# Performance work log

Measured on AMD Instinct MI355X. Metric: run time of the kernel, lower is better.

## Reference

```python
import jax, jax.numpy as jnp
import numpy as np

N, E = 50000, 800000
D, DE = 128, 64
BN_EPS = 1e-5


def _bn(h, gamma, beta):
    # BatchNorm1d in training mode: biased batch statistics over the node axis
    mu = jnp.mean(h, axis=0)
    var = jnp.var(h, axis=0)
    return (h - mu) * jax.lax.rsqrt(var + BN_EPS) * gamma + beta


def setup_inputs() -> dict:
    key = jax.random.key(0)
    ks = jax.random.split(key, 12)
    s = lambda d: 1.0 / np.sqrt(d)
    return {
        "x": jax.random.normal(ks[0], (N, D), jnp.float32),
        "edge_index": jax.random.randint(ks[1], (2, E), 0, N, jnp.int64),
        "edge_attr_processed": jax.random.normal(ks[2], (E, DE), jnp.float32),
        # GINEConv edge linear: edge_dim -> node_dim
        "We": jax.random.uniform(ks[3], (D, DE), jnp.float32, -s(DE), s(DE)),
        "be": jnp.zeros((D,), jnp.float32),
        # MLP: Linear(D, 2D) -> BN(2D) -> ReLU -> Linear(2D, D)
        "W1": jax.random.uniform(ks[4], (2 * D, D), jnp.float32, -s(D), s(D)),
        "b1": jnp.zeros((2 * D,), jnp.float32),
        "g1": jnp.ones((2 * D,), jnp.float32),
        "beta1": jnp.zeros((2 * D,), jnp.float32),
        "W2": jax.random.uniform(ks[5], (D, 2 * D), jnp.float32, -s(2 * D), s(2 * D)),
        "b2": jnp.zeros((D,), jnp.float32),
        # outer BatchNorm(D)
        "g2": jnp.ones((D,), jnp.float32),
        "beta2": jnp.zeros((D,), jnp.float32),
        # GINE trainable eps (init 0.0)
        "eps": jnp.zeros((), jnp.float32),
    }


def reference(x, edge_index, edge_attr_processed, We, be, W1, b1, g1, beta1,
              W2, b2, g2, beta2, eps):
    src, dst = edge_index[0], edge_index[1]
    # GINEConv message: ReLU(x_j + Lin(edge_attr)); gather + edge add + relu
    msg = jax.nn.relu(x[src] + edge_attr_processed @ We.T + be)  # [E, D]
    # scatter-add aggregation at destination nodes
    agg = jax.ops.segment_sum(msg, dst, num_segments=x.shape[0])  # [N, D]
    h = (1.0 + eps) * x + agg
    # MLP: Linear -> BN -> ReLU -> Linear
    h = jax.nn.relu(_bn(h @ W1.T + b1, g1, beta1)) @ W2.T + b2
    # outer BN -> ReLU (dropout is identity at inference)
    return jax.nn.relu(_bn(h, g2, beta2))
```

## Files before the change

kernel.cpp:

```cpp
#include <hip/hip_runtime.h>
#include <stdint.h>
#include <stddef.h>


#define NN 50000
#define EE 800000
#define DD 128
#define DE 64
#define H1 256
#define NGRP 3125

typedef __attribute__((ext_vector_type(8))) short short8;
typedef __attribute__((ext_vector_type(4))) float floatx4;

__device__ __forceinline__ short f2bf(float f) {
    union { float f; uint32_t u; } v; v.f = f;
    return (short)((v.u + 0x7FFFu + ((v.u >> 16) & 1u)) >> 16);
}
__device__ __forceinline__ float bf2f(uint16_t u) {
    union { uint32_t u; float f; } v; v.u = (uint32_t)u << 16;
    return v.f;
}

__global__ __launch_bounds__(256) void swz_all_kernel(
    const float* __restrict__ We, const float* __restrict__ W1,
    const float* __restrict__ W2, short* __restrict__ dst) {
    int idx = blockIdx.x * 256 + threadIdx.x;
    if (idx >= 73728) return;
    const float* src; int KC, K, local; short* dp; bool perm = false;
    if (idx < 8192)       { src = We; KC = 2; K = 64;  local = idx;          dp = dst; }
    else if (idx < 40960) { src = W1; KC = 4; K = 128; local = idx - 8192;  dp = dst + 8192; perm = true; }
    else                  { src = W2; KC = 8; K = 256; local = idx - 40960; dp = dst + 40960; }
    int j = local & 7;
    int lane = (local >> 3) & 63;
    int f = local >> 9;
    int kc = f % KC;
    int nt = f / KC;
    int n = nt * 16 + (lane & 15);
    int k = kc * 32 + ((lane >> 4) & 3) * 8 + j;
    if (perm) k = ((k & 7) << 4) | (k >> 3);
    dp[local] = f2bf(src[(size_t)n * K + k]);
}

__global__ __launch_bounds__(256) void count_kernel(const int* __restrict__ ei,
                                                    uint32_t* __restrict__ deg) {
    int e = blockIdx.x * 256 + threadIdx.x;
    atomicAdd(&deg[ei[EE + e]], 1u);
}

__global__ __launch_bounds__(256) void scan1_kernel(const uint32_t* __restrict__ deg,
                                                    uint32_t* __restrict__ partial) {
    __shared__ uint32_t ls[256];
    int i = blockIdx.x * 256 + threadIdx.x;
    ls[threadIdx.x] = deg[i];
    __syncthreads();
    for (int s = 128; s > 0; s >>= 1) {
        if (threadIdx.x < s) ls[threadIdx.x] += ls[threadIdx.x + s];
        __syncthreads();
    }
    if (threadIdx.x == 0) partial[blockIdx.x] = ls[0];
}

__global__ __launch_bounds__(256) void scan2_kernel(uint32_t* __restrict__ partial) {
    __shared__ uint32_t ls[196];
    if (threadIdx.x < 196) ls[threadIdx.x] = partial[threadIdx.x];
    __syncthreads();
    if (threadIdx.x == 0) {
        uint32_t run = 0;
        for (int i = 0; i < 196; ++i) { uint32_t t = ls[i]; ls[i] = run; run += t; }
    }
    __syncthreads();
    if (threadIdx.x < 196) partial[threadIdx.x] = ls[threadIdx.x];
}

__global__ __launch_bounds__(256) void scan3_kernel(const uint32_t* __restrict__ deg,
                                                    const uint32_t* __restrict__ partial,
                                                    uint32_t* __restrict__ base,
                                                    uint32_t* __restrict__ cursor) {
    __shared__ uint32_t ls[256];
    int i = blockIdx.x * 256 + threadIdx.x;
    uint32_t v = (i < NN) ? deg[i] : 0u;
    ls[threadIdx.x] = v;
    __syncthreads();
    for (int off = 1; off < 256; off <<= 1) {
        uint32_t t = (threadIdx.x >= off) ? ls[threadIdx.x - off] : 0u;
        __syncthreads();
        ls[threadIdx.x] += t;
        __syncthreads();
    }
    if (i < NN) {
        uint32_t b = partial[blockIdx.x] + ls[threadIdx.x] - v;
        base[i] = b;
        cursor[i] = b;
    } else if (i == NN) {
        base[NN] = EE;
    }
}

__global__ __launch_bounds__(256) void pos_kernel(const int* __restrict__ ei,
                                                  uint32_t* __restrict__ cursor,
                                                  uint32_t* __restrict__ pos) {
    int e = blockIdx.x * 256 + threadIdx.x;
    pos[e] = atomicAdd(&cursor[ei[EE + e]], 1u);
}

#define EDGE_GPW 5
__global__ __launch_bounds__(256) void edge_kernel(
    const float* __restrict__ x,
    const int* __restrict__ ei,
    const float* __restrict__ ea,
    const short* __restrict__ weswz,
    const float* __restrict__ be,
    const uint32_t* __restrict__ pos,
    uint16_t* __restrict__ msg)
{
    const int wave = threadIdx.x >> 6;
    const int lane = threadIdx.x & 63;
    const int l16 = lane & 15;
    const int q = lane >> 4;

    const short8* wp = (const short8*)weswz;
    short8 bfr[16];
#pragma unroll
    for (int f = 0; f < 16; ++f) bfr[f] = wp[f * 64 + lane];
    float bev[8];
#pragma unroll
    for (int t = 0; t < 8; ++t) bev[t] = be[t * 16 + l16];

    const int gbase = (blockIdx.x * 4 + wave) * EDGE_GPW;
    for (int g = 0; g < EDGE_GPW; ++g) {
        const int e0 = (gbase + g) * 16;
        const float* earow = ea + (size_t)(e0 + l16) * DE + q * 8;
        floatx4 p0 = *(const floatx4*)(earow);
        floatx4 p1 = *(const floatx4*)(earow + 4);
        floatx4 p2 = *(const floatx4*)(earow + 32);
        floatx4 p3 = *(const floatx4*)(earow + 36);
        short8 af0, af1;
#pragma unroll
        for (int j = 0; j < 4; ++j) {
            af0[j]     = f2bf(p0[j]);
            af0[j + 4] = f2bf(p1[j]);
            af1[j]     = f2bf(p2[j]);
            af1[j + 4] = f2bf(p3[j]);
        }
        floatx4 acc[8];
#pragma unroll
        for (int t = 0; t < 8; ++t) {
            floatx4 z = {0.f, 0.f, 0.f, 0.f};
            z = __builtin_amdgcn_mfma_f32_16x16x32_bf16(af0, bfr[t * 2], z, 0, 0, 0);
            acc[t] = __builtin_amdgcn_mfma_f32_16x16x32_bf16(af1, bfr[t * 2 + 1], z, 0, 0, 0);
        }
        int   sidx[4];
        uint32_t ppv[4];
#pragma unroll
        for (int r = 0; r < 4; ++r) {
            sidx[r] = ei[e0 + q * 4 + r];
            ppv[r]  = pos[e0 + q * 4 + r];
        }
#pragma unroll
        for (int r = 0; r < 4; ++r) {
            const float* xr = x + (size_t)sidx[r] * DD + l16;
            uint32_t pk[4];
#pragma unroll
            for (int tt = 0; tt < 4; ++tt) {
                float v0 = fmaxf(acc[2 * tt][r]     + bev[2 * tt]     + xr[(2 * tt) * 16], 0.f);
                float v1 = fmaxf(acc[2 * tt + 1][r] + bev[2 * tt + 1] + xr[(2 * tt + 1) * 16], 0.f);
                pk[tt] = (uint32_t)(uint16_t)f2bf(v0) | ((uint32_t)(uint16_t)f2bf(v1) << 16);
            }
            uint4 val = {pk[0], pk[1], pk[2], pk[3]};
            *(uint4*)(msg + (size_t)ppv[r] * DD + l16 * 8) = val;
        }
    }
}

__global__ __launch_bounds__(256) void reduce_kernel(
    const uint16_t* __restrict__ msg,
    const uint32_t* __restrict__ basep,
    const float* __restrict__ x,
    const float* __restrict__ epsp,
    uint16_t* __restrict__ hbf)
{
    const int n = blockIdx.x * 4 + (threadIdx.x >> 6);
    const int lane = threadIdx.x & 63;
    const uint32_t b0 = basep[n];
    const uint32_t d = basep[n + 1] - b0;
    const uint32_t* mp = (const uint32_t*)msg + (size_t)b0 * 64 + lane;
    float s0a = 0.f, s1a = 0.f, s0b = 0.f, s1b = 0.f;
    float s0c = 0.f, s1c = 0.f, s0d = 0.f, s1d = 0.f;
    uint32_t i = 0;
    for (; i + 4 <= d; i += 4) {
        uint32_t u0 = mp[(size_t)(i + 0) * 64];
        uint32_t u1 = mp[(size_t)(i + 1) * 64];
        uint32_t u2 = mp[(size_t)(i + 2) * 64];
        uint32_t u3 = mp[(size_t)(i + 3) * 64];
        s0a += bf2f((uint16_t)(u0 & 0xFFFFu)); s1a += bf2f((uint16_t)(u0 >> 16));
        s0b += bf2f((uint16_t)(u1 & 0xFFFFu)); s1b += bf2f((uint16_t)(u1 >> 16));
        s0c += bf2f((uint16_t)(u2 & 0xFFFFu)); s1c += bf2f((uint16_t)(u2 >> 16));
        s0d += bf2f((uint16_t)(u3 & 0xFFFFu)); s1d += bf2f((uint16_t)(u3 >> 16));
    }
    for (; i < d; ++i) {
        uint32_t u = mp[(size_t)i * 64];
        s0a += bf2f((uint16_t)(u & 0xFFFFu)); s1a += bf2f((uint16_t)(u >> 16));
    }
    float s0 = (s0a + s0b) + (s0c + s0d);
    float s1 = (s1a + s1b) + (s1c + s1d);
    const float c1 = 1.0f + epsp[0];
    const int o0 = (((lane * 2) & 7) << 4) + (lane >> 2);
    const float* xrow = x + (size_t)n * DD;
    float xa = xrow[o0];
    float xb = xrow[o0 + 16];
    uint32_t pk = (uint32_t)(uint16_t)f2bf(c1 * xa + s0) |
                  ((uint32_t)(uint16_t)f2bf(c1 * xb + s1) << 16);
    ((uint32_t*)hbf)[n * 64 + lane] = pk;
}

__global__ __launch_bounds__(256) void gemm1_kernel(
    const uint16_t* __restrict__ hbf,
    const short* __restrict__ w1swz,
    const float* __restrict__ b1,
    uint16_t* __restrict__ t1,
    float* __restrict__ gsum,
    float* __restrict__ gsq)
{
    __shared__ float ls[H1];
    __shared__ float ls2[H1];
    const int tid = threadIdx.x;
    ls[tid] = 0.f; ls2[tid] = 0.f;
    __syncthreads();

    const int wave = tid >> 6;
    const int lane = tid & 63;
    const int l16 = lane & 15;
    const int q = lane >> 4;
    const short8* wp = (const short8*)w1swz;

    const int grp = blockIdx.x * 4 + wave;
    if (grp < NGRP) {
        const int n0 = grp * 16;
        const uint16_t* hr = hbf + (size_t)(n0 + l16) * DD + q * 8;
        short8 af[4];
#pragma unroll
        for (int kc = 0; kc < 4; ++kc) af[kc] = *(const short8*)(hr + kc * 32);
#pragma unroll
        for (int nt = 0; nt < 16; ++nt) {
            floatx4 acc = {0.f, 0.f, 0.f, 0.f};
#pragma unroll
            for (int kc = 0; kc < 4; ++kc)
                acc = __builtin_amdgcn_mfma_f32_16x16x32_bf16(
                    af[kc], wp[(nt * 4 + kc) * 64 + lane], acc, 0, 0, 0);
            const float bb = b1[nt * 16 + l16];
            float s = 0.f, s2 = 0.f;
#pragma unroll
            for (int r = 0; r < 4; ++r) {
                float v = acc[r] + bb;
                t1[(size_t)(n0 + q * 4 + r) * H1 + nt * 16 + l16] = (uint16_t)f2bf(v);
                s += v; s2 += v * v;
            }
            atomicAdd(&ls[nt * 16 + l16], s);
            atomicAdd(&ls2[nt * 16 + l16], s2);
        }
    }
    __syncthreads();
    atomicAdd(&gsum[tid], ls[tid]);
    atomicAdd(&gsq[tid], ls2[tid]);
}

__global__ __launch_bounds__(256) void gemm2_kernel(
    const uint16_t* __restrict__ t1,
    const float* __restrict__ scale1,
    const float* __restrict__ shift1,
    const short* __restrict__ w2swz,
    const float* __restrict__ b2,
    uint16_t* __restrict__ h2,
    float* __restrict__ gsum,
    float* __restrict__ gsq)
{
    __shared__ float ls[DD];
    __shared__ float ls2[DD];
    const int tid = threadIdx.x;
    if (tid < DD) { ls[tid] = 0.f; ls2[tid] = 0.f; }
    __syncthreads();

    const int wave = tid >> 6;
    const int lane = tid & 63;
    const int l16 = lane & 15;
    const int q = lane >> 4;
    const short8* wp = (const short8*)w2swz;

    const int grp = blockIdx.x * 4 + wave;
    if (grp < NGRP) {
        const int n0 = grp * 16;
        const uint16_t* tr = t1 + (size_t)(n0 + l16) * H1 + q * 8;
        floatx4 acc[8];
#pragma unroll
        for (int nt = 0; nt < 8; ++nt) acc[nt] = (floatx4){0.f, 0.f, 0.f, 0.f};
#pragma unroll
        for (int kc = 0; kc < 8; ++kc) {
            short8 tv = *(const short8*)(tr + kc * 32);
            const int kb = kc * 32 + q * 8;
            short8 af;
#pragma unroll
            for (int j = 0; j < 8; ++j) {
                float u = bf2f((uint16_t)tv[j]) * scale1[kb + j] + shift1[kb + j];
                af[j] = f2bf(fmaxf(u, 0.f));
            }
#pragma unroll
            for (int nt = 0; nt < 8; ++nt)
                acc[nt] = __builtin_amdgcn_mfma_f32_16x16x32_bf16(
                    af, wp[(nt * 8 + kc) * 64 + lane], acc[nt], 0, 0, 0);
        }
#pragma unroll
        for (int nt = 0; nt < 8; ++nt) {
            const float bb = b2[nt * 16 + l16];
            float s = 0.f, s2 = 0.f;
#pragma unroll
            for (int r = 0; r < 4; ++r) {
                float v = acc[nt][r] + bb;
                h2[(size_t)(n0 + q * 4 + r) * DD + nt * 16 + l16] = (uint16_t)f2bf(v);
                s += v; s2 += v * v;
            }
            atomicAdd(&ls[nt * 16 + l16], s);
            atomicAdd(&ls2[nt * 16 + l16], s2);
        }
    }
    __syncthreads();
    if (tid < DD) {
        atomicAdd(&gsum[tid], ls[tid]);
        atomicAdd(&gsq[tid], ls2[tid]);
    }
}

__global__ void finalize_kernel(const float* __restrict__ ssum,
                                const float* __restrict__ ssumsq,
                                const float* __restrict__ gamma,
                                const float* __restrict__ beta,
                                float* __restrict__ scale,
                                float* __restrict__ shift, int C) {
    int c = threadIdx.x;
    if (c >= C) return;
    float mu = ssum[c] * (1.0f / NN);
    float var = ssumsq[c] * (1.0f / NN) - mu * mu;
    float rs = rsqrtf(var + 1e-5f);
    float sc = gamma[c] * rs;
    scale[c] = sc;
    shift[c] = beta[c] - mu * sc;
}

__global__ __launch_bounds__(256) void out_kernel(const uint16_t* __restrict__ h2,
                                                  const float* __restrict__ scale2,
                                                  const float* __restrict__ shift2,
                                                  float* __restrict__ out) {
    int idx = blockIdx.x * 256 + threadIdx.x;
    int base = idx * 8;
    int c = base & (DD - 1);
    uint4 pk = *(const uint4*)(h2 + base);
    const uint32_t u[4] = {pk.x, pk.y, pk.z, pk.w};
    floatx4 o0, o1;
#pragma unroll
    for (int j = 0; j < 4; ++j) {
        float vlo = bf2f((uint16_t)(u[j] & 0xFFFFu));
        float vhi = bf2f((uint16_t)(u[j] >> 16));
        int cc = c + j * 2;
        float a = fmaxf(vlo * scale2[cc] + shift2[cc], 0.f);
        float b = fmaxf(vhi * scale2[cc + 1] + shift2[cc + 1], 0.f);
        if (j < 2) { o0[j * 2] = a; o0[j * 2 + 1] = b; }
        else       { o1[(j - 2) * 2] = a; o1[(j - 2) * 2 + 1] = b; }
    }
    *(floatx4*)(out + base) = o0;
    *(floatx4*)(out + base + 4) = o1;
}

extern "C" void kernel_launch(void* const* d_in, const int* in_sizes, int n_in,
                              void* d_out, int out_size, void* d_ws, size_t ws_size,
                              hipStream_t stream) {
    const float* x     = (const float*)d_in[0];
    const int*   ei    = (const int*)d_in[1];
    const float* ea    = (const float*)d_in[2];
    const float* We    = (const float*)d_in[3];
    const float* be    = (const float*)d_in[4];
    const float* W1    = (const float*)d_in[5];
    const float* b1    = (const float*)d_in[6];
    const float* g1    = (const float*)d_in[7];
    const float* beta1 = (const float*)d_in[8];
    const float* W2    = (const float*)d_in[9];
    const float* b2    = (const float*)d_in[10];
    const float* g2    = (const float*)d_in[11];
    const float* beta2 = (const float*)d_in[12];
    const float* epsp  = (const float*)d_in[13];

    float* ws      = (float*)d_ws;
    float* gsum1   = ws + 0;
    float* gsq1    = ws + 256;
    float* gsum2   = ws + 512;
    float* gsq2    = ws + 640;
    float* scale1  = ws + 768;
    float* shift1  = ws + 1024;
    float* scale2  = ws + 1280;
    float* shift2  = ws + 1408;
    uint32_t* deg     = (uint32_t*)(ws + 1536);
    uint32_t* basep   = deg + 50176;
    uint32_t* cursor  = basep + 50432;
    uint32_t* partial = cursor + 50176;
    uint32_t* pos     = partial + 256;
    uint16_t* hbf     = (uint16_t*)(pos + EE);
    uint16_t* msg     = hbf + (size_t)NN * DD;
    uint16_t* t1      = msg;
    uint16_t* h2      = t1 + (size_t)NN * H1;
    short*    wswz    = (short*)(msg + (size_t)EE * DD);
    short*    weswz   = wswz;
    short*    w1swz   = wswz + 8192;
    short*    w2swz   = wswz + 40960;

    hipMemsetAsync(ws, 0, (1536 + 50176) * sizeof(uint32_t), stream);

    swz_all_kernel<<<dim3(288), 256, 0, stream>>>(We, W1, W2, wswz);
    count_kernel<<<dim3(3125), 256, 0, stream>>>(ei, deg);
    scan1_kernel<<<dim3(196), 256, 0, stream>>>(deg, partial);
    scan2_kernel<<<dim3(1), 256, 0, stream>>>(partial);
    scan3_kernel<<<dim3(196), 256, 0, stream>>>(deg, partial, basep, cursor);
    pos_kernel<<<dim3(3125), 256, 0, stream>>>(ei, cursor, pos);

    edge_kernel<<<dim3(2500), 256, 0, stream>>>(x, ei, ea, weswz, be, pos, msg);
    reduce_kernel<<<dim3(12500), 256, 0, stream>>>(msg, basep, x, epsp, hbf);

    gemm1_kernel<<<dim3(782), 256, 0, stream>>>(hbf, w1swz, b1, t1, gsum1, gsq1);
    finalize_kernel<<<dim3(1), 256, 0, stream>>>(gsum1, gsq1, g1, beta1, scale1, shift1, H1);

    gemm2_kernel<<<dim3(782), 256, 0, stream>>>(t1, scale1, shift1, w2swz, b2, h2, gsum2, gsq2);
    finalize_kernel<<<dim3(1), 128, 0, stream>>>(gsum2, gsq2, g2, beta2, scale2, shift2, DD);

    out_kernel<<<dim3(3125), 256, 0, stream>>>(h2, scale2, shift2, (float*)d_out);
}
```

Baseline: 613.7 us.

## Remap edge feature layout for vectorized x gathers and 16-byte message reduction

Changes the We swizzle so each lane owns 8 contiguous output features. The edge kernel can then gather x rows with two float4 loads instead of eight strided scalar loads. It also prefetches the next group's source indices and fully unrolls the group loop. The reduce kernel now reads messages as uint4 (four edges per wave step across quarter-waves) and combines partials with cross-lane shuffles, with the W1 input permutation removed to match the new hbf layout. This adds shuffle work and relies on the layout staying consistent across the swizzle, edge and reduce kernels.

```diff
diff --git a/kernel.cpp b/kernel.cpp
--- a/kernel.cpp
+++ b/kernel.cpp
@@ -27,18 +27,17 @@
     const float* __restrict__ W2, short* __restrict__ dst) {
     int idx = blockIdx.x * 256 + threadIdx.x;
     if (idx >= 73728) return;
-    const float* src; int KC, K, local; short* dp; bool perm = false;
-    if (idx < 8192)       { src = We; KC = 2; K = 64;  local = idx;          dp = dst; }
-    else if (idx < 40960) { src = W1; KC = 4; K = 128; local = idx - 8192;  dp = dst + 8192; perm = true; }
+    const float* src; int KC, K, local; short* dp; bool efeat = false;
+    if (idx < 8192)       { src = We; KC = 2; K = 64;  local = idx;          dp = dst; efeat = true; }
+    else if (idx < 40960) { src = W1; KC = 4; K = 128; local = idx - 8192;  dp = dst + 8192; }
     else                  { src = W2; KC = 8; K = 256; local = idx - 40960; dp = dst + 40960; }
     int j = local & 7;
     int lane = (local >> 3) & 63;
     int f = local >> 9;
     int kc = f % KC;
     int nt = f / KC;
-    int n = nt * 16 + (lane & 15);
+    int n = efeat ? ((lane & 15) * 8 + nt) : (nt * 16 + (lane & 15));
     int k = kc * 32 + ((lane >> 4) & 3) * 8 + j;
-    if (perm) k = ((k & 7) << 4) | (k >> 3);
     dp[local] = f2bf(src[(size_t)n * K + k]);
 }
 
@@ -123,13 +122,33 @@
     short8 bfr[16];
 #pragma unroll
     for (int f = 0; f < 16; ++f) bfr[f] = wp[f * 64 + lane];
-    float bev[8];
-#pragma unroll
-    for (int t = 0; t < 8; ++t) bev[t] = be[t * 16 + l16];
+    floatx4 bv0 = *(const floatx4*)(be + l16 * 8);
+    floatx4 bv1 = *(const floatx4*)(be + l16 * 8 + 4);
 
     const int gbase = (blockIdx.x * 4 + wave) * EDGE_GPW;
+    int sidx[4];
+#pragma unroll
+    for (int r = 0; r < 4; ++r) sidx[r] = ei[gbase * 16 + q * 4 + r];
+
+#pragma unroll
     for (int g = 0; g < EDGE_GPW; ++g) {
         const int e0 = (gbase + g) * 16;
+        floatx4 xa[4], xb[4];
+#pragma unroll
+        for (int r = 0; r < 4; ++r) {
+            const float* xr = x + (size_t)sidx[r] * DD + l16 * 8;
+            xa[r] = *(const floatx4*)(xr);
+            xb[r] = *(const floatx4*)(xr + 4);
+        }
+        int sidxn[4];
+        if (g + 1 < EDGE_GPW) {
+#pragma unroll
+            for (int r = 0; r < 4; ++r) sidxn[r] = ei[e0 + 16 + q * 4 + r];
+        }
+        uint32_t ppv[4];
+#pragma unroll
+        for (int r = 0; r < 4; ++r) ppv[r] = pos[e0 + q * 4 + r];
+
         const float* earow = ea + (size_t)(e0 + l16) * DE + q * 8;
         floatx4 p0 = *(const floatx4*)(earow);
         floatx4 p1 = *(const floatx4*)(earow + 4);
@@ -150,28 +169,34 @@
             z = __builtin_amdgcn_mfma_f32_16x16x32_bf16(af0, bfr[t * 2], z, 0, 0, 0);
             acc[t] = __builtin_amdgcn_mfma_f32_16x16x32_bf16(af1, bfr[t * 2 + 1], z, 0, 0, 0);
         }
-        int   sidx[4];
-        uint32_t ppv[4];
 #pragma unroll
         for (int r = 0; r < 4; ++r) {
-            sidx[r] = ei[e0 + q * 4 + r];
-            ppv[r]  = pos[e0 + q * 4 + r];
-        }
-#pragma unroll
-        for (int r = 0; r < 4; ++r) {
-            const float* xr = x + (size_t)sidx[r] * DD + l16;
             uint32_t pk[4];
 #pragma unroll
             for (int tt = 0; tt < 4; ++tt) {
-                float v0 = fmaxf(acc[2 * tt][r]     + bev[2 * tt]     + xr[(2 * tt) * 16], 0.f);
-                float v1 = fmaxf(acc[2 * tt + 1][r] + bev[2 * tt + 1] + xr[(2 * tt + 1) * 16], 0.f);
+                float X0 = (tt < 2) ? xa[r][2 * tt]     : xb[r][2 * tt - 4];
+                float X1 = (tt < 2) ? xa[r][2 * tt + 1] : xb[r][2 * tt - 3];
+                float B0 = (tt < 2) ? bv0[2 * tt]       : bv1[2 * tt - 4];
+                float B1 = (tt < 2) ? bv0[2 * tt + 1]   : bv1[2 * tt - 3];
+                float v0 = fmaxf(acc[2 * tt][r]     + B0 + X0, 0.f);
+                float v1 = fmaxf(acc[2 * tt + 1][r] + B1 + X1, 0.f);
                 pk[tt] = (uint32_t)(uint16_t)f2bf(v0) | ((uint32_t)(uint16_t)f2bf(v1) << 16);
             }
             uint4 val = {pk[0], pk[1], pk[2], pk[3]};
             *(uint4*)(msg + (size_t)ppv[r] * DD + l16 * 8) = val;
         }
-    }
-}
+        if (g + 1 < EDGE_GPW) {
+#pragma unroll
+            for (int r = 0; r < 4; ++r) sidx[r] = sidxn[r];
+        }
+    }
+}
+
+#define ACC8(u) do { \
+    s0 += bf2f((uint16_t)((u).x & 0xFFFFu)); s1 += bf2f((uint16_t)((u).x >> 16)); \
+    s2 += bf2f((uint16_t)((u).y & 0xFFFFu)); s3 += bf2f((uint16_t)((u).y >> 16)); \
+    s4 += bf2f((uint16_t)((u).z & 0xFFFFu)); s5 += bf2f((uint16_t)((u).z >> 16)); \
+    s6 += bf2f((uint16_t)((u).w & 0xFFFFu)); s7 += bf2f((uint16_t)((u).w >> 16)); } while (0)
 
 __global__ __launch_bounds__(256) void reduce_kernel(
     const uint16_t* __restrict__ msg,
@@ -182,36 +207,38 @@
 {
     const int n = blockIdx.x * 4 + (threadIdx.x >> 6);
     const int lane = threadIdx.x & 63;
+    const int l16 = lane & 15;
+    const int q = lane >> 4;
     const uint32_t b0 = basep[n];
     const uint32_t d = basep[n + 1] - b0;
-    const uint32_t* mp = (const uint32_t*)msg + (size_t)b0 * 64 + lane;
-    float s0a = 0.f, s1a = 0.f, s0b = 0.f, s1b = 0.f;
-    float s0c = 0.f, s1c = 0.f, s0d = 0.f, s1d = 0.f;
+    const uint4* bp = (const uint4*)((const uint32_t*)msg + (size_t)b0 * 64) + lane;
+    float s0 = 0.f, s1 = 0.f, s2 = 0.f, s3 = 0.f;
+    float s4 = 0.f, s5 = 0.f, s6 = 0.f, s7 = 0.f;
+    const uint32_t nb = d >> 2;
+    const uint32_t rem = d & 3u;
     uint32_t i = 0;
-    for (; i + 4 <= d; i += 4) {
-        uint32_t u0 = mp[(size_t)(i + 0) * 64];
-        uint32_t u1 = mp[(size_t)(i + 1) * 64];
-        uint32_t u2 = mp[(size_t)(i + 2) * 64];
-        uint32_t u3 = mp[(size_t)(i + 3) * 64];
-        s0a += bf2f((uint16_t)(u0 & 0xFFFFu)); s1a += bf2f((uint16_t)(u0 >> 16));
-        s0b += bf2f((uint16_t)(u1 & 0xFFFFu)); s1b += bf2f((uint16_t)(u1 >> 16));
-        s0c += bf2f((uint16_t)(u2 & 0xFFFFu)); s1c += bf2f((uint16_t)(u2 >> 16));
-        s0d += bf2f((uint16_t)(u3 & 0xFFFFu)); s1d += bf2f((uint16_t)(u3 >> 16));
-    }
-    for (; i < d; ++i) {
-        uint32_t u = mp[(size_t)i * 64];
-        s0a += bf2f((uint16_t)(u & 0xFFFFu)); s1a += bf2f((uint16_t)(u >> 16));
-    }
-    float s0 = (s0a + s0b) + (s0c + s0d);
-    float s1 = (s1a + s1b) + (s1c + s1d);
+    for (; i + 2 <= nb; i += 2) {
+        uint4 a = bp[(size_t)i * 64];
+        uint4 b = bp[(size_t)(i + 1) * 64];
+        ACC8(a); ACC8(b);
+    }
+    if (i < nb) { uint4 a = bp[(size_t)i * 64]; ACC8(a); }
+    if ((uint32_t)q < rem) { uint4 a = bp[(size_t)nb * 64]; ACC8(a); }
+    s0 += __shfl_xor(s0, 16); s0 += __shfl_xor(s0, 32);
+    s1 += __shfl_xor(s1, 16); s1 += __shfl_xor(s1, 32);
+    s2 += __shfl_xor(s2, 16); s2 += __shfl_xor(s2, 32);
+    s3 += __shfl_xor(s3, 16); s3 += __shfl_xor(s3, 32);
+    s4 += __shfl_xor(s4, 16); s4 += __shfl_xor(s4, 32);
+    s5 += __shfl_xor(s5, 16); s5 += __shfl_xor(s5, 32);
+    s6 += __shfl_xor(s6, 16); s6 += __shfl_xor(s6, 32);
+    s7 += __shfl_xor(s7, 16); s7 += __shfl_xor(s7, 32);
     const float c1 = 1.0f + epsp[0];
-    const int o0 = (((lane * 2) & 7) << 4) + (lane >> 2);
-    const float* xrow = x + (size_t)n * DD;
-    float xa = xrow[o0];
-    float xb = xrow[o0 + 16];
-    uint32_t pk = (uint32_t)(uint16_t)f2bf(c1 * xa + s0) |
-                  ((uint32_t)(uint16_t)f2bf(c1 * xb + s1) << 16);
-    ((uint32_t*)hbf)[n * 64 + lane] = pk;
+    const float2 xv = *(const float2*)(x + (size_t)n * DD + (l16 * 4 + q) * 2);
+    float a0 = (q == 0) ? s0 : (q == 1) ? s2 : (q == 2) ? s4 : s6;
+    float a1 = (q == 0) ? s1 : (q == 1) ? s3 : (q == 2) ? s5 : s7;
+    uint32_t pk = (uint32_t)(uint16_t)f2bf(c1 * xv.x + a0) |
+                  ((uint32_t)(uint16_t)f2bf(c1 * xv.y + a1) << 16);
+    ((uint32_t*)hbf)[(size_t)n * 64 + l16 * 4 + q] = pk;
 }
 
 __global__ __launch_bounds__(256) void gemm1_kernel(
```

Measured after the change: 611.5 us. About the same (-0.4%).
